# Kernel optimization log

Measured on AMD Instinct MI355X. Metric: run time of the kernel, lower is better.

## Reference

```python
import jax, jax.numpy as jnp
import numpy as np

# Levelized timing graph: L levels of P pins, each pin at level l>0 has K fanin
# arcs from level l-1. src_idx holds level-local source pin indices.
L = 32          # logic depth
P = 131072      # pins per level  (n_pins = L*P = 4,194,304)
K = 2           # fanin arcs per pin
N_NETS = 1000000
TIMING_PERIOD = jnp.float32(10.0)
NEG = jnp.float32(-1e30)
POS = jnp.float32(1e30)


def setup_inputs() -> dict:
    key = jax.random.key(0)
    k1, k2, k3, k4 = jax.random.split(key, 4)
    # per-pin arc delays (ns-scale)
    pin_delays = jax.random.uniform(k1, (L * P,), dtype=jnp.float32) * 0.5
    # fanin sources: level-local indices into the previous level
    src_idx = jax.random.randint(k2, (L - 1, P, K), 0, P, dtype=jnp.int32)
    # net id of each timing arc
    net_ids = jax.random.randint(k3, (L - 1, P, K), 0, N_NETS, dtype=jnp.int32)
    net_mask_ignore_large = jax.random.uniform(k4, (N_NETS,)) < 0.01
    return {
        "pin_delays": pin_delays,
        "src_idx": src_idx,
        "net_ids": net_ids,
        "net_mask_ignore_large": net_mask_ignore_large,
    }


def reference(pin_delays, src_idx, net_ids, net_mask_ignore_large):
    delays = pin_delays.reshape(L, P)              # [L, P]
    valid = ~net_mask_ignore_large[net_ids]        # [L-1, P, K] arcs on ignored nets are skipped

    # ---- forward (arrival) propagation: max over fanin ----
    arr = [delays[0]]                              # source pins launch at their own delay
    for l in range(1, L):
        contrib = arr[-1][src_idx[l - 1]] + delays[l][:, None]   # [P, K]
        contrib = jnp.where(valid[l - 1], contrib, NEG)
        arr.append(jnp.maximum(jnp.max(contrib, axis=-1), delays[l]))
    arrival = jnp.stack(arr)                       # [L, P]

    # ---- backward (required) propagation: min over fanout (scatter-min) ----
    req = [None] * L
    req[L - 1] = jnp.full((P,), TIMING_PERIOD, dtype=jnp.float32)  # endpoints
    for l in range(L - 2, -1, -1):
        contrib = req[l + 1] - delays[l + 1]                        # [P]
        c = jnp.where(valid[l], contrib[:, None], POS)              # [P, K]
        r = jnp.full((P,), TIMING_PERIOD, dtype=jnp.float32)
        r = r.at[src_idx[l].ravel()].min(c.ravel())
        req[l] = r
    required = jnp.stack(req)                      # [L, P]

    pin_arrivals = arrival.reshape(-1)
    pin_requires = required.reshape(-1)
    pin_slacks = pin_requires - pin_arrivals
    return pin_arrivals, pin_requires, pin_slacks, net_mask_ignore_large
```

## Files before the change

kernel.cpp:

```cpp
#include <hip/hip_runtime.h>

constexpr int L = 32;
constexpr int P = 131072;
constexpr int LP = L * P;
constexpr int NNETS = 1000000;
constexpr int NBLK = 2048;
constexpr int TPB = 256;
constexpr int NTHR = NBLK * TPB;
constexpr float TPER = 10.0f;
constexpr float NEGV = -1e30f;
constexpr int WS_BITS = 0;
constexpr int WS_CNT1 = 32768;
constexpr int WS_CNT2 = 33808;
constexpr int WS_FLAG = 33840;
constexpr int WS_ZERO_BEG = 32768;
constexpr int WS_ZERO_END = 33856;

__device__ __forceinline__ float agent_load_f(const float* p) {
  return __hip_atomic_load(p, __ATOMIC_RELAXED, __HIP_MEMORY_SCOPE_AGENT);
}
__device__ __forceinline__ void agent_store_f(float* p, float v) {
  __hip_atomic_store(p, v, __ATOMIC_RELAXED, __HIP_MEMORY_SCOPE_AGENT);
}

__device__ __forceinline__ void atomic_min_f32(float* addr, float val) {
  if (val >= 0.0f) {
    atomicMin(reinterpret_cast<int*>(addr), __float_as_int(val));
  } else {
    atomicMax(reinterpret_cast<unsigned int*>(addr), __float_as_uint(val));
  }
}

__device__ __forceinline__ void gbar(int* ws, int epoch) {
  asm volatile("s_waitcnt vmcnt(0)" ::: "memory");
  __syncthreads();
  if (threadIdx.x == 0) {
    int* flag = ws + WS_FLAG;
    int* cnt1 = ws + WS_CNT1 + ((blockIdx.x >> 5) << 4);
    int o1 = __hip_atomic_fetch_add(cnt1, 1, __ATOMIC_RELAXED,
                                    __HIP_MEMORY_SCOPE_AGENT);
    if (o1 == epoch * 32 - 1) {
      int o2 = __hip_atomic_fetch_add(ws + WS_CNT2, 1, __ATOMIC_RELAXED,
                                      __HIP_MEMORY_SCOPE_AGENT);
      if (o2 == epoch * 64 - 1)
        __hip_atomic_store(flag, epoch, __ATOMIC_RELAXED,
                           __HIP_MEMORY_SCOPE_AGENT);
    }
    while (__hip_atomic_load(flag, __ATOMIC_RELAXED,
                             __HIP_MEMORY_SCOPE_AGENT) < epoch) {
      __builtin_amdgcn_s_sleep(2);
    }
  }
  __syncthreads();
}

__global__ __launch_bounds__(TPB, 8) void sta_persist(
    const float* __restrict__ delays, const int* __restrict__ src,
    const int* __restrict__ net, const int* __restrict__ mask,
    float* __restrict__ out, int* __restrict__ ws) {
  const int t = blockIdx.x * TPB + threadIdx.x;
  const int lane = threadIdx.x & 63;
  float* arr = out;
  float* req = out + LP;
  float* slk = out + 2 * LP;
  float* mf = out + 3 * LP;
  int* bits = ws + WS_BITS;

#pragma unroll
  for (int j = 0; j < 2; ++j) {
    const int idx = j * NTHR + t;
    int mv = 0;
    if (idx < NNETS) mv = mask[idx];
    unsigned long long bal = __ballot(mv != 0);
    if (lane == 0) {
      const int word = (j * NTHR + (t & ~63)) >> 5;
      __hip_atomic_store(reinterpret_cast<unsigned long long*>(bits + word),
                         bal, __ATOMIC_RELAXED, __HIP_MEMORY_SCOPE_AGENT);
    }
  }
  {
    const int idx = t * 2;
    if (idx < NNETS) {
      const int2 m = *reinterpret_cast<const int2*>(mask + idx);
      float2 f = {m.x ? 1.0f : 0.0f, m.y ? 1.0f : 0.0f};
      *reinterpret_cast<float2*>(mf + idx) = f;
    }
  }
  if (t < P) agent_store_f(arr + t, delays[t]);
#pragma unroll
  for (int c = 0; c < 8; ++c) agent_store_f(req + c * NTHR + t, TPER);
  gbar(ws, 1);

  const int half = t >> 18;
  const int a = t & (2 * P - 1);
  const int p = a >> 1;

  for (int i = 1; i < L; ++i) {
    if (half == 0) {
      const int lf = i;
      const float d = delays[lf * P + p];
      const int s = src[(size_t)(lf - 1) * 2 * P + a];
      const int n = net[(size_t)(lf - 1) * 2 * P + a];
      float v = arr[(size_t)(lf - 1) * P + s] + d;
      if ((bits[n >> 5] >> (n & 31)) & 1) v = NEGV;
      const float vo = __shfl_xor(v, 1);
      if ((a & 1) == 0)
        agent_store_f(arr + (size_t)lf * P + p, fmaxf(fmaxf(v, vo), d));
    } else {
      const int lb = L - 1 - i;
      float c0 = 0.0f;
      if ((a & 1) == 0)
        c0 = agent_load_f(req + (size_t)(lb + 1) * P + p) -
             delays[(lb + 1) * P + p];
      const float c = __shfl(c0, lane & 62);
      const int s = src[(size_t)lb * 2 * P + a];
      const int n = net[(size_t)lb * 2 * P + a];
      if (!((bits[n >> 5] >> (n & 31)) & 1))
        atomic_min_f32(req + (size_t)lb * P + s, c);
    }
    gbar(ws, i + 1);
  }

#pragma unroll
  for (int c = 0; c < 8; ++c) {
    const int idx = c * NTHR + t;
    const float av = arr[idx];
    const float rv = agent_load_f(req + idx);
    slk[idx] = rv - av;
  }
}

__global__ __launch_bounds__(256) void sta_init(
    const float* __restrict__ delays, const int* __restrict__ mask,
    float* __restrict__ out) {
  int i4 = (blockIdx.x * blockDim.x + threadIdx.x) * 4;
  if (i4 < LP) {
    float4 ten = {TPER, TPER, TPER, TPER};
    *reinterpret_cast<float4*>(out + LP + i4) = ten;
    if (i4 < P)
      *reinterpret_cast<float4*>(out + i4) =
          *reinterpret_cast<const float4*>(delays + i4);
  }
  if (i4 < NNETS) {
    int4 m = *reinterpret_cast<const int4*>(mask + i4);
    float4 f = {(float)(m.x != 0), (float)(m.y != 0), (float)(m.z != 0),
                (float)(m.w != 0)};
    *reinterpret_cast<float4*>(out + 3 * LP + i4) = f;
  }
}

__global__ __launch_bounds__(256) void sta_step_direct(
    const float* __restrict__ delays, const int* __restrict__ src,
    const int* __restrict__ net, const int* __restrict__ mask,
    float* __restrict__ out, int i) {
  const int p = blockIdx.x * blockDim.x + threadIdx.x;
  float* arr = out;
  float* req = out + LP;
  const int lf = i, lb = L - 1 - i;
  {
    const float d = delays[lf * P + p];
    const int2 s = *reinterpret_cast<const int2*>(src + (size_t)(lf - 1) * P * 2 + p * 2);
    const int2 n = *reinterpret_cast<const int2*>(net + (size_t)(lf - 1) * P * 2 + p * 2);
    const float* ap = arr + (lf - 1) * P;
    const float v0 = mask[n.x] ? NEGV : ap[s.x] + d;
    const float v1 = mask[n.y] ? NEGV : ap[s.y] + d;
    arr[lf * P + p] = fmaxf(fmaxf(v0, v1), d);
  }
  {
    const float c = req[(lb + 1) * P + p] - delays[(lb + 1) * P + p];
    const int2 s = *reinterpret_cast<const int2*>(src + (size_t)lb * P * 2 + p * 2);
    const int2 n = *reinterpret_cast<const int2*>(net + (size_t)lb * P * 2 + p * 2);
    float* rp = req + lb * P;
    if (!mask[n.x]) atomic_min_f32(rp + s.x, c);
    if (!mask[n.y]) atomic_min_f32(rp + s.y, c);
  }
}

__global__ __launch_bounds__(256) void sta_slack(float* __restrict__ out) {
  int i4 = (blockIdx.x * blockDim.x + threadIdx.x) * 4;
  if (i4 < LP) {
    float4 a = *reinterpret_cast<const float4*>(out + i4);
    float4 r = *reinterpret_cast<const float4*>(out + LP + i4);
    float4 s = {r.x - a.x, r.y - a.y, r.z - a.z, r.w - a.w};
    *reinterpret_cast<float4*>(out + 2 * LP + i4) = s;
  }
}

extern "C" void kernel_launch(void* const* d_in, const int* in_sizes, int n_in,
                              void* d_out, int out_size, void* d_ws, size_t ws_size,
                              hipStream_t stream) {
  const float* delays = (const float*)d_in[0];
  const int* src = (const int*)d_in[1];
  const int* net = (const int*)d_in[2];
  const int* mask = (const int*)d_in[3];
  float* out = (float*)d_out;
  int* ws = (int*)d_ws;

  if (ws_size >= (size_t)WS_ZERO_END * sizeof(int)) {
    hipMemsetAsync((char*)d_ws + (size_t)WS_ZERO_BEG * sizeof(int), 0,
                   (size_t)(WS_ZERO_END - WS_ZERO_BEG) * sizeof(int), stream);
    void* args[] = {(void*)&delays, (void*)&src, (void*)&net,
                    (void*)&mask, (void*)&out, (void*)&ws};
    hipError_t e = hipLaunchCooperativeKernel((const void*)sta_persist,
                                              dim3(NBLK), dim3(TPB), args, 0,
                                              stream);
    if (e == hipSuccess) return;
    (void)hipGetLastError();
  }
  sta_init<<<LP / 1024, 256, 0, stream>>>(delays, mask, out);
  for (int i = 1; i < L; ++i)
    sta_step_direct<<<P / 256, 256, 0, stream>>>(delays, src, net, mask, out, i);
  sta_slack<<<LP / 1024, 256, 0, stream>>>(out);
}
```

Baseline: 631.2 us.

## Pre-encode ignore mask into source indices and pad required array to spread atomics

Two pre-kernels are added before the persistent kernel. One builds the net-ignore bitmask, and the other folds each arc's ignore bit into the sign bit of its source index. This removes the per-level net-id loads and bitmask lookups. The required-time scatter-min now targets a workspace array with an 8-float stride per pin, which spreads atomics across more cache lines to cut contention. Results are copied back to the output at the end. The cost is two extra launches, a full pass over src/net each call, and a large strided workspace that uses bandwidth poorly on the loads and init stores.

```diff
diff --git a/kernel.cpp b/kernel.cpp
--- a/kernel.cpp
+++ b/kernel.cpp
@@ -3,18 +3,23 @@
 constexpr int L = 32;
 constexpr int P = 131072;
 constexpr int LP = L * P;
+constexpr int NARC = (L - 1) * P * 2;
 constexpr int NNETS = 1000000;
 constexpr int NBLK = 2048;
 constexpr int TPB = 256;
 constexpr int NTHR = NBLK * TPB;
 constexpr float TPER = 10.0f;
 constexpr float NEGV = -1e30f;
-constexpr int WS_BITS = 0;
-constexpr int WS_CNT1 = 32768;
-constexpr int WS_CNT2 = 33808;
-constexpr int WS_FLAG = 33840;
-constexpr int WS_ZERO_BEG = 32768;
-constexpr int WS_ZERO_END = 33856;
+constexpr int SRCMASK = P - 1;
+constexpr int RSTR = 8;
+
+constexpr size_t WS_RQP = 0;
+constexpr size_t WS_ESRC = WS_RQP + (size_t)LP * RSTR;
+constexpr size_t WS_BITS = WS_ESRC + NARC;
+constexpr size_t WS_CNT1 = WS_BITS + 32768;
+constexpr size_t WS_CNT2 = WS_CNT1 + 1024 + 16;
+constexpr size_t WS_FLAG = WS_CNT2 + 16;
+constexpr size_t WS_END = WS_FLAG + 16;
 
 __device__ __forceinline__ float agent_load_f(const float* p) {
   return __hip_atomic_load(p, __ATOMIC_RELAXED, __HIP_MEMORY_SCOPE_AGENT);
@@ -54,30 +59,55 @@
   __syncthreads();
 }
 
-__global__ __launch_bounds__(TPB, 8) void sta_persist(
-    const float* __restrict__ delays, const int* __restrict__ src,
-    const int* __restrict__ net, const int* __restrict__ mask,
-    float* __restrict__ out, int* __restrict__ ws) {
+__global__ __launch_bounds__(TPB) void sta_bits(const int* __restrict__ mask,
+                                                int* __restrict__ ws) {
   const int t = blockIdx.x * TPB + threadIdx.x;
   const int lane = threadIdx.x & 63;
-  float* arr = out;
-  float* req = out + LP;
-  float* slk = out + 2 * LP;
-  float* mf = out + 3 * LP;
   int* bits = ws + WS_BITS;
-
 #pragma unroll
   for (int j = 0; j < 2; ++j) {
     const int idx = j * NTHR + t;
     int mv = 0;
     if (idx < NNETS) mv = mask[idx];
     unsigned long long bal = __ballot(mv != 0);
-    if (lane == 0) {
-      const int word = (j * NTHR + (t & ~63)) >> 5;
-      __hip_atomic_store(reinterpret_cast<unsigned long long*>(bits + word),
-                         bal, __ATOMIC_RELAXED, __HIP_MEMORY_SCOPE_AGENT);
-    }
-  }
+    if (lane == 0)
+      *reinterpret_cast<unsigned long long*>(bits +
+                                             ((j * NTHR + (t & ~63)) >> 5)) = bal;
+  }
+}
+
+__global__ __launch_bounds__(256) void sta_esrc(const int* __restrict__ src,
+                                                const int* __restrict__ net,
+                                                int* __restrict__ ws) {
+  const int a4 = (blockIdx.x * blockDim.x + threadIdx.x) * 4;
+  const int* bits = ws + WS_BITS;
+  if (a4 < NARC) {
+    int4 s = *reinterpret_cast<const int4*>(src + a4);
+    int4 n = *reinterpret_cast<const int4*>(net + a4);
+    s.x |= ((bits[n.x >> 5] >> (n.x & 31)) & 1) << 31;
+    s.y |= ((bits[n.y >> 5] >> (n.y & 31)) & 1) << 31;
+    s.z |= ((bits[n.z >> 5] >> (n.z & 31)) & 1) << 31;
+    s.w |= ((bits[n.w >> 5] >> (n.w & 31)) & 1) << 31;
+    *reinterpret_cast<int4*>(ws + WS_ESRC + a4) = s;
+  }
+}
+
+__global__ __launch_bounds__(TPB, 8) void sta_persist(
+    const float* __restrict__ delays, const int* __restrict__ mask,
+    float* __restrict__ out, int* __restrict__ ws) {
+  const int t = blockIdx.x * TPB + threadIdx.x;
+  const int lane = threadIdx.x & 63;
+  float* arr = out;
+  float* reqo = out + LP;
+  float* slk = out + 2 * LP;
+  float* mf = out + 3 * LP;
+  float* rqp = reinterpret_cast<float*>(ws + WS_RQP);
+  const int* esrc = ws + WS_ESRC;
+
+  if (t < P) agent_store_f(arr + t, delays[t]);
+#pragma unroll
+  for (int c = 0; c < 8; ++c)
+    agent_store_f(rqp + (size_t)(c * NTHR + t) * RSTR, TPER);
   {
     const int idx = t * 2;
     if (idx < NNETS) {
@@ -86,9 +116,6 @@
       *reinterpret_cast<float2*>(mf + idx) = f;
     }
   }
-  if (t < P) agent_store_f(arr + t, delays[t]);
-#pragma unroll
-  for (int c = 0; c < 8; ++c) agent_store_f(req + c * NTHR + t, TPER);
   gbar(ws, 1);
 
   const int half = t >> 18;
@@ -99,10 +126,9 @@
     if (half == 0) {
       const int lf = i;
       const float d = delays[lf * P + p];
-      const int s = src[(size_t)(lf - 1) * 2 * P + a];
-      const int n = net[(size_t)(lf - 1) * 2 * P + a];
-      float v = arr[(size_t)(lf - 1) * P + s] + d;
-      if ((bits[n >> 5] >> (n & 31)) & 1) v = NEGV;
+      const int s = esrc[(size_t)(lf - 1) * 2 * P + a];
+      float v = arr[(size_t)(lf - 1) * P + (s & SRCMASK)] + d;
+      if (s < 0) v = NEGV;
       const float vo = __shfl_xor(v, 1);
       if ((a & 1) == 0)
         agent_store_f(arr + (size_t)lf * P + p, fmaxf(fmaxf(v, vo), d));
@@ -110,13 +136,12 @@
       const int lb = L - 1 - i;
       float c0 = 0.0f;
       if ((a & 1) == 0)
-        c0 = agent_load_f(req + (size_t)(lb + 1) * P + p) -
+        c0 = agent_load_f(rqp + ((size_t)(lb + 1) * P + p) * RSTR) -
              delays[(lb + 1) * P + p];
       const float c = __shfl(c0, lane & 62);
-      const int s = src[(size_t)lb * 2 * P + a];
-      const int n = net[(size_t)lb * 2 * P + a];
-      if (!((bits[n >> 5] >> (n & 31)) & 1))
-        atomic_min_f32(req + (size_t)lb * P + s, c);
+      const int s = esrc[(size_t)lb * 2 * P + a];
+      if (s >= 0)
+        atomic_min_f32(rqp + ((size_t)lb * P + s) * RSTR, c);
     }
     gbar(ws, i + 1);
   }
@@ -124,8 +149,9 @@
 #pragma unroll
   for (int c = 0; c < 8; ++c) {
     const int idx = c * NTHR + t;
+    const float rv = agent_load_f(rqp + (size_t)idx * RSTR);
     const float av = arr[idx];
-    const float rv = agent_load_f(req + idx);
+    reqo[idx] = rv;
     slk[idx] = rv - av;
   }
 }
@@ -196,11 +222,12 @@
   float* out = (float*)d_out;
   int* ws = (int*)d_ws;
 
-  if (ws_size >= (size_t)WS_ZERO_END * sizeof(int)) {
-    hipMemsetAsync((char*)d_ws + (size_t)WS_ZERO_BEG * sizeof(int), 0,
-                   (size_t)(WS_ZERO_END - WS_ZERO_BEG) * sizeof(int), stream);
-    void* args[] = {(void*)&delays, (void*)&src, (void*)&net,
-                    (void*)&mask, (void*)&out, (void*)&ws};
+  if (ws_size >= WS_END * sizeof(int)) {
+    hipMemsetAsync((char*)d_ws + WS_CNT1 * sizeof(int), 0,
+                   (WS_END - WS_CNT1) * sizeof(int), stream);
+    sta_bits<<<NBLK, TPB, 0, stream>>>(mask, ws);
+    sta_esrc<<<NARC / 4 / 256, 256, 0, stream>>>(src, net, ws);
+    void* args[] = {(void*)&delays, (void*)&mask, (void*)&out, (void*)&ws};
     hipError_t e = hipLaunchCooperativeKernel((const void*)sta_persist,
                                               dim3(NBLK), dim3(TPB), args, 0,
                                               stream);
```

New measurement: 721.7 us. 1.14x slower.
